# Performance work log

Hardware: AMD Instinct MI355X
Metric: run time of the kernel (lower is better)

## Reference

```python
import jax, jax.numpy as jnp
import numpy as np

B, S, H, E, K = 4, 4096, 1024, 8, 2
DFF = 4 * H


def setup_inputs() -> dict:
    key = jax.random.key(0)
    ks = jax.random.split(key, 6)
    s_in = 1.0 / np.sqrt(H)
    s_ff = 1.0 / np.sqrt(DFF)
    return {
        "x": jax.random.normal(ks[0], (B, S, H), dtype=jnp.float32),
        "router_w": jax.random.normal(ks[1], (E, H), dtype=jnp.float32) * s_in,
        "router_b": jnp.zeros((E,), dtype=jnp.float32),
        "fc1_w": jax.random.normal(ks[2], (E, DFF, H), dtype=jnp.float32) * s_in,
        "fc1_b": jnp.zeros((E, DFF), dtype=jnp.float32),
        "fc2_w": jax.random.normal(ks[3], (E, H, DFF), dtype=jnp.float32) * s_ff,
        "fc2_b": jnp.zeros((E, H), dtype=jnp.float32),
    }


def reference(x, router_w, router_b, fc1_w, fc1_b, fc2_w, fc2_b):
    b, s, h = x.shape
    e = router_w.shape[0]
    k = K
    # Router: [B,S,E]
    logits = jnp.einsum("bsh,eh->bse", x, router_w) + router_b
    top_v, top_i = jax.lax.top_k(logits, k)            # [B,S,K]
    probs = jax.nn.softmax(top_v, axis=-1)             # softmax over top-k logits
    # Combine weights per expert [B,S,E]; top-k indices are distinct per token,
    # so summing one-hot*prob over k matches the original's gather-of-first-match.
    combine = jnp.sum(jax.nn.one_hot(top_i, e, dtype=x.dtype) * probs[..., None], axis=-2)
    xf = x.reshape(-1, h)            # [T,H], T = B*S
    cf = combine.reshape(-1, e)      # [T,E]
    out = jnp.zeros_like(xf)
    for ei in range(e):              # fixed small loop over experts
        hdn = jax.nn.relu(xf @ fc1_w[ei].T + fc1_b[ei])   # [T,4H]
        y = hdn @ fc2_w[ei].T + fc2_b[ei]                 # [T,H]
        out = out + cf[:, ei:ei + 1] * y                  # zero weight == not routed
    return out.reshape(b, s, h)
```

## Files before the change

### kernel.cpp

```cpp
#include <hip/hip_runtime.h>
#include <stdint.h>

#define T_TOKENS 16384
#define H_DIM 1024
#define E_NUM 8
#define DFF_DIM 4096

#define BMT 128
#define BNT 128
#define BKT 64
#define MT_CAP 264
#define PAD_ROWS (MT_CAP * BMT)
#define NCHUNK 4
#define MT_PER_CHUNK (MT_CAP / NCHUNK)
#define CHUNK_ROWS (MT_PER_CHUNK * BMT)

#define WS_COUNTS     0
#define WS_CURSOR     32
#define WS_OFFS       64
#define WS_SLOT_TOK   256
#define WS_SLOT_W     135424
#define WS_EIDX       270592
#define WS_EW         401664
#define WS_WC1        532736
#define WS_WC2        67641600
#define WS_XB         134750464
#define WS_HDN        168304896
#define WS_OUTK1      237510912
#define WS_REQUIRED   271065344UL
#define WS_SMALL_ZERO 270592

typedef __attribute__((ext_vector_type(8))) short short8;
typedef __attribute__((ext_vector_type(4))) float f32x4;

__device__ __forceinline__ unsigned short f2bf(float f) {
  union { float f; unsigned int u; } v; v.f = f;
  unsigned int r = v.u + 0x7FFFu + ((v.u >> 16) & 1u);
  return (unsigned short)(r >> 16);
}

__device__ __forceinline__ float bf2f(unsigned short b) {
  union { unsigned int u; float f; } v; v.u = ((unsigned int)b) << 16;
  return v.f;
}

__device__ __forceinline__ void load_lds16(const void* g, void* l) {
  __builtin_amdgcn_global_load_lds(
      (const __attribute__((address_space(1))) void*)g,
      (__attribute__((address_space(3))) void*)l, 16, 0, 0);
}

#define CONV_BLOCKS 2048
__global__ __launch_bounds__(256) void convert_weights(
    const float* __restrict__ w1, const float* __restrict__ w2,
    unsigned short* __restrict__ wc1, unsigned short* __restrict__ wc2) {
  const int total4 = (E_NUM * DFF_DIM * H_DIM) / 4;
  const int step = CONV_BLOCKS * 256;
  for (int i = blockIdx.x * 256 + threadIdx.x; i < total4; i += step) {
    float4 a = ((const float4*)w1)[i];
    float4 b = ((const float4*)w2)[i];
    ushort4 ua, ub;
    ua.x = f2bf(a.x); ua.y = f2bf(a.y); ua.z = f2bf(a.z); ua.w = f2bf(a.w);
    ub.x = f2bf(b.x); ub.y = f2bf(b.y); ub.z = f2bf(b.z); ub.w = f2bf(b.w);
    ((ushort4*)wc1)[i] = ua;
    ((ushort4*)wc2)[i] = ub;
  }
}

__global__ __launch_bounds__(256) void router_kernel(
    const float* __restrict__ x, const float* __restrict__ rw,
    const float* __restrict__ rb, unsigned short* __restrict__ xb,
    int* __restrict__ eidx, float* __restrict__ ew) {
  __shared__ float4 rws[E_NUM * 256];
  const int tid = threadIdx.x;
#pragma unroll
  for (int k = 0; k < 8; ++k) rws[k * 256 + tid] = ((const float4*)rw)[k * 256 + tid];
  __syncthreads();

  const int wave = tid >> 6;
  const int lane = tid & 63;
#pragma unroll
  for (int i = 0; i < 4; ++i) {
    const int t = blockIdx.x * 16 + wave * 4 + i;
    const float4* xrow = (const float4*)(x + (size_t)t * H_DIM);
    float4 xv[4];
#pragma unroll
    for (int j = 0; j < 4; ++j) xv[j] = xrow[j * 64 + lane];

    ushort4* xbrow = (ushort4*)(xb + (size_t)t * H_DIM);
#pragma unroll
    for (int j = 0; j < 4; ++j) {
      ushort4 o;
      o.x = f2bf(xv[j].x); o.y = f2bf(xv[j].y);
      o.z = f2bf(xv[j].z); o.w = f2bf(xv[j].w);
      xbrow[j * 64 + lane] = o;
    }

    float s[E_NUM];
#pragma unroll
    for (int e = 0; e < E_NUM; ++e) {
      float a = 0.f;
#pragma unroll
      for (int j = 0; j < 4; ++j) {
        float4 wv = rws[e * 256 + j * 64 + lane];
        a += xv[j].x * wv.x + xv[j].y * wv.y + xv[j].z * wv.z + xv[j].w * wv.w;
      }
      s[e] = a;
    }
#pragma unroll
    for (int off = 32; off; off >>= 1) {
#pragma unroll
      for (int e = 0; e < E_NUM; ++e) s[e] += __shfl_xor(s[e], off);
    }
    if (lane == 0) {
      float lg[E_NUM];
#pragma unroll
      for (int e = 0; e < E_NUM; ++e) lg[e] = s[e] + rb[e];
      int i0 = 0; float m0 = lg[0];
#pragma unroll
      for (int e = 1; e < E_NUM; ++e)
        if (lg[e] > m0) { m0 = lg[e]; i0 = e; }
      int i1 = -1; float m1 = -3.4e38f;
#pragma unroll
      for (int e = 0; e < E_NUM; ++e)
        if (e != i0 && lg[e] > m1) { m1 = lg[e]; i1 = e; }
      float e1 = expf(m1 - m0);
      float denom = 1.f + e1;
      ((int2*)eidx)[t] = make_int2(i0, i1);
      ((float2*)ew)[t] = make_float2(1.f / denom, e1 / denom);
    }
  }
}

__global__ __launch_bounds__(1024) void count_kernel(const int* __restrict__ eidx,
                                                     int* __restrict__ counts,
                                                     int* __restrict__ offs,
                                                     int* __restrict__ cursor) {
  __shared__ int hist[E_NUM];
  const int tid = threadIdx.x;
  const int lane = tid & 63;
  if (tid < E_NUM) hist[tid] = 0;
  __syncthreads();
  int c[E_NUM];
#pragma unroll
  for (int e = 0; e < E_NUM; ++e) c[e] = 0;
  const int4* p = (const int4*)eidx;
#pragma unroll
  for (int i = 0; i < 8; ++i) {
    int4 v = p[i * 1024 + tid];
#pragma unroll
    for (int e = 0; e < E_NUM; ++e)
      c[e] += (v.x == e) + (v.y == e) + (v.z == e) + (v.w == e);
  }
#pragma unroll
  for (int off = 32; off; off >>= 1) {
#pragma unroll
    for (int e = 0; e < E_NUM; ++e) c[e] += __shfl_xor(c[e], off);
  }
  if (lane == 0) {
#pragma unroll
    for (int e = 0; e < E_NUM; ++e) atomicAdd(&hist[e], c[e]);
  }
  __syncthreads();
  if (tid == 0) {
    int acc = 0;
    offs[0] = 0;
#pragma unroll
    for (int e = 0; e < E_NUM; ++e) {
      counts[e] = hist[e];
      cursor[e] = 0;
      acc += ((hist[e] + BMT - 1) / BMT) * BMT;
      offs[e + 1] = acc;
    }
  }
}

__global__ __launch_bounds__(1024) void scatter_kernel(
    const int* __restrict__ eidx, const float* __restrict__ ew,
    const int* __restrict__ offs, int* __restrict__ cursor,
    int* __restrict__ slot_token, float* __restrict__ slot_w) {
  __shared__ int wcnt[16][E_NUM];
  __shared__ int wpre[16][E_NUM];
  __shared__ int bbase[E_NUM];
  __shared__ int soffs[E_NUM];
  const int tid = threadIdx.x, w = tid >> 6, lane = tid & 63;
  const int t = blockIdx.x * 1024 + tid;
  const int2 epair = ((const int2*)eidx)[t];
  const float2 wpair = ((const float2*)ew)[t];
  const int e0 = epair.x, e1 = epair.y;
  const unsigned long long lt = (1ULL << lane) - 1ULL;
  if (tid < E_NUM) soffs[tid] = offs[tid];
  int r0 = 0, r1 = 0;
#pragma unroll
  for (int e = 0; e < E_NUM; ++e) {
    unsigned long long m0 = __ballot(e0 == e);
    unsigned long long m1 = __ballot(e1 == e);
    int c0 = __popcll(m0);
    if (e0 == e) r0 = __popcll(m0 & lt);
    if (e1 == e) r1 = c0 + __popcll(m1 & lt);
    if (lane == 0) wcnt[w][e] = c0 + __popcll(m1);
  }
  __syncthreads();
  if (tid < E_NUM) {
    int run = 0;
#pragma unroll
    for (int w2 = 0; w2 < 16; ++w2) {
      wpre[w2][tid] = run;
      run += wcnt[w2][tid];
    }
    bbase[tid] = atomicAdd(&cursor[tid], run);
  }
  __syncthreads();
  const int s0 = soffs[e0] + bbase[e0] + wpre[w][e0] + r0;
  const int s1 = soffs[e1] + bbase[e1] + wpre[w][e1] + r1;
  slot_token[s0] = t;
  slot_w[s0] = wpair.x;
  slot_token[s1] = t | (int)0x80000000;
  slot_w[s1] = wpair.y;
}

template <int KTOT>
__device__ __forceinline__ void gemm_core(const unsigned short* const* aptr,
                                          const unsigned short* const* bptr,
                                          unsigned short* lA, unsigned short* lB,
                                          f32x4 acc[4][4]) {
  const int tid = threadIdx.x;
  const int w = tid >> 6, lane = tid & 63;
  const int wm = w >> 1, wn = w & 1;
  const int rrow = lane & 15;
  const int rq = lane >> 4;

  for (int ks = 0; ks < KTOT / BKT; ++ks) {
    const int k0 = ks * BKT;
#pragma unroll
    for (int i = 0; i < 4; ++i) {
      load_lds16(aptr[i] + k0, lA + i * 2048 + w * 512);
      load_lds16(bptr[i] + k0, lB + i * 2048 + w * 512);
    }
    __syncthreads();
#pragma unroll
    for (int kk = 0; kk < 2; ++kk) {
      short8 af[4], bfr[4];
#pragma unroll
      for (int mi = 0; mi < 4; ++mi)
        af[mi] = *(const short8*)(lA + (wm * 64 + mi * 16 + rrow) * BKT + kk * 32 + rq * 8);
#pragma unroll
      for (int ni = 0; ni < 4; ++ni)
        bfr[ni] = *(const short8*)(lB + (wn * 64 + ni * 16 + rrow) * BKT + kk * 32 + rq * 8);
#pragma unroll
      for (int mi = 0; mi < 4; ++mi)
#pragma unroll
        for (int ni = 0; ni < 4; ++ni)
          acc[mi][ni] = __builtin_amdgcn_mfma_f32_16x16x32_bf16(af[mi], bfr[ni], acc[mi][ni], 0, 0, 0);
    }
    __syncthreads();
  }
}

__global__ __launch_bounds__(256, 2) void fc1_kernel(
    const unsigned short* __restrict__ xb, const unsigned short* __restrict__ wc1,
    const float* __restrict__ fc1_b, const int* __restrict__ offs,
    const int* __restrict__ counts, const int* __restrict__ slot_token,
    unsigned short* __restrict__ hdn, int chunk) {
  __shared__ unsigned short sA[BMT * BKT];
  __shared__ unsigned short sB[BNT * BKT];
  const int mt = chunk * MT_PER_CHUNK + blockIdx.y;
  const int row0 = mt * BMT;
  if (row0 >= offs[E_NUM]) return;
  int e = 0;
#pragma unroll
  for (int i = 1; i < E_NUM; ++i) e = (row0 >= offs[i]) ? i : e;
  const int n0 = blockIdx.x * BNT;

  f32x4 acc[4][4];
  f32x4 zf = {0.f, 0.f, 0.f, 0.f};
#pragma unroll
  for (int mi = 0; mi < 4; ++mi)
#pragma unroll
    for (int ni = 0; ni < 4; ++ni) acc[mi][ni] = zf;

  const int tid = threadIdx.x;
  const int srow = tid >> 3;
  const int scol = (tid & 7) * 8;
  const unsigned short* Bm = wc1 + (size_t)e * DFF_DIM * H_DIM + (size_t)n0 * H_DIM;
  const unsigned short* aptr[4];
  const unsigned short* bptr[4];
#pragma unroll
  for (int i = 0; i < 4; ++i) {
    const int r = i * 32 + srow;
    const int tok = slot_token[row0 + r] & 0x7FFFFFFF;
    aptr[i] = xb + (size_t)tok * H_DIM + scol;
    bptr[i] = Bm + (size_t)r * H_DIM + scol;
  }
  gemm_core<H_DIM>(aptr, bptr, sA, sB, acc);

  const int w = tid >> 6;
  const int lane = tid & 63;
  const int wm = w >> 1, wn = w & 1;
  const int rrow = lane & 15, rq = lane >> 4;
  const int cnt = counts[e];
  const int lbase = row0 - offs[e];
  const int hrow0 = row0 - chunk * CHUNK_ROWS;
#pragma unroll
  for (int mi = 0; mi < 4; ++mi) {
#pragma unroll
    for (int j = 0; j < 4; ++j) {
      const int rit = wm * 64 + mi * 16 + rq * 4 + j;
      if (lbase + rit >= cnt) continue;
      unsigned short* hrow = hdn + (size_t)(hrow0 + rit) * DFF_DIM;
#pragma unroll
      for (int ni = 0; ni < 4; ++ni) {
        const int n = n0 + wn * 64 + ni * 16 + rrow;
        float v = acc[mi][ni][j] + fc1_b[e * DFF_DIM + n];
        v = v > 0.f ? v : 0.f;
        hrow[n] = f2bf(v);
      }
    }
  }
}

__global__ __launch_bounds__(256, 2) void fc2_kernel(
    const unsigned short* __restrict__ hdn, const unsigned short* __restrict__ wc2,
    const float* __restrict__ fc2_b, const int* __restrict__ offs,
    const int* __restrict__ counts, const int* __restrict__ slot_token,
    const float* __restrict__ slot_w, float* __restrict__ out,
    unsigned short* __restrict__ outk1, int chunk) {
  __shared__ unsigned short sA[BMT * BKT];
  __shared__ unsigned short sB[BNT * BKT];
  const int id = blockIdx.x;
  const int xcd = id & 7, j = id >> 3;
  int ml, nt;
  if (j < 64) { ml = xcd * 8 + (j & 7); nt = j >> 3; }
  else        { ml = 64 + (j & 1);      nt = xcd;    }
  const int mt = chunk * MT_PER_CHUNK + ml;
  const int row0 = mt * BMT;
  if (row0 >= offs[E_NUM]) return;
  int e = 0;
#pragma unroll
  for (int i = 1; i < E_NUM; ++i) e = (row0 >= offs[i]) ? i : e;
  const int n0 = nt * BNT;

  f32x4 acc[4][4];
  f32x4 zf = {0.f, 0.f, 0.f, 0.f};
#pragma unroll
  for (int mi = 0; mi < 4; ++mi)
#pragma unroll
    for (int ni = 0; ni < 4; ++ni) acc[mi][ni] = zf;

  const int tid = threadIdx.x;
  const int srow = tid >> 3;
  const int scol = (tid & 7) * 8;
  const unsigned short* A = hdn + (size_t)(ml * BMT) * DFF_DIM;
  const unsigned short* Bm = wc2 + (size_t)e * H_DIM * DFF_DIM + (size_t)n0 * DFF_DIM;
  const unsigned short* aptr[4];
  const unsigned short* bptr[4];
#pragma unroll
  for (int i = 0; i < 4; ++i) {
    const int r = i * 32 + srow;
    aptr[i] = A + (size_t)r * DFF_DIM + scol;
    bptr[i] = Bm + (size_t)r * DFF_DIM + scol;
  }
  gemm_core<DFF_DIM>(aptr, bptr, sA, sB, acc);

  const int w = tid >> 6;
  const int lane = tid & 63;
  const int wm = w >> 1, wn = w & 1;
  const int rrow = lane & 15, rq = lane >> 4;
  const int cnt = counts[e];
  const int lbase = row0 - offs[e];
#pragma unroll
  for (int mi = 0; mi < 4; ++mi) {
#pragma unroll
    for (int j2 = 0; j2 < 4; ++j2) {
      const int rit = wm * 64 + mi * 16 + rq * 4 + j2;
      if (lbase + rit >= cnt) continue;
      const int gr = row0 + rit;
      const int st = slot_token[gr];
      const int tok = st & 0x7FFFFFFF;
      const float wgt = slot_w[gr];
#pragma unroll
      for (int ni = 0; ni < 4; ++ni) {
        const int h = n0 + wn * 64 + ni * 16 + rrow;
        const float v = (acc[mi][ni][j2] + fc2_b[e * H_DIM + h]) * wgt;
        if (st >= 0) out[(size_t)tok * H_DIM + h] = v;
        else         outk1[(size_t)tok * H_DIM + h] = f2bf(v);
      }
    }
  }
}

__global__ __launch_bounds__(256) void add_kernel(
    float* __restrict__ out, const unsigned short* __restrict__ outk1) {
  const int wave = threadIdx.x >> 6;
  const int lane = threadIdx.x & 63;
  const int t = blockIdx.x * 4 + wave;
  float4* orow = (float4*)(out + (size_t)t * H_DIM);
  const ushort4* krow = (const ushort4*)(outk1 + (size_t)t * H_DIM);
#pragma unroll
  for (int j = 0; j < 4; ++j) {
    const int idx = j * 64 + lane;
    float4 a = orow[idx];
    ushort4 b = krow[idx];
    a.x += bf2f(b.x); a.y += bf2f(b.y); a.z += bf2f(b.z); a.w += bf2f(b.w);
    orow[idx] = a;
  }
}

extern "C" void kernel_launch(void* const* d_in, const int* in_sizes, int n_in,
                              void* d_out, int out_size, void* d_ws, size_t ws_size,
                              hipStream_t stream) {
  const float* x        = (const float*)d_in[0];
  const float* router_w = (const float*)d_in[1];
  const float* router_b = (const float*)d_in[2];
  const float* fc1_w    = (const float*)d_in[3];
  const float* fc1_b    = (const float*)d_in[4];
  const float* fc2_w    = (const float*)d_in[5];
  const float* fc2_b    = (const float*)d_in[6];
  float* out = (float*)d_out;

  char* ws = (char*)d_ws;
  int* counts            = (int*)(ws + WS_COUNTS);
  int* cursor            = (int*)(ws + WS_CURSOR);
  int* offs              = (int*)(ws + WS_OFFS);
  int* slot_token        = (int*)(ws + WS_SLOT_TOK);
  float* slot_w          = (float*)(ws + WS_SLOT_W);
  int* eidx              = (int*)(ws + WS_EIDX);
  float* ew              = (float*)(ws + WS_EW);
  unsigned short* wc1    = (unsigned short*)(ws + WS_WC1);
  unsigned short* wc2    = (unsigned short*)(ws + WS_WC2);
  unsigned short* xb     = (unsigned short*)(ws + WS_XB);
  unsigned short* hdn    = (unsigned short*)(ws + WS_HDN);
  unsigned short* outk1  = (unsigned short*)(ws + WS_OUTK1);

  if (ws_size < WS_REQUIRED) {
    hipMemsetAsync(d_out, 0, (size_t)T_TOKENS * H_DIM * sizeof(float), stream);
    return;
  }
  hipMemsetAsync(ws, 0, WS_SMALL_ZERO, stream);

  convert_weights<<<CONV_BLOCKS, 256, 0, stream>>>(fc1_w, fc2_w, wc1, wc2);
  router_kernel<<<T_TOKENS / 16, 256, 0, stream>>>(x, router_w, router_b, xb, eidx, ew);
  count_kernel<<<1, 1024, 0, stream>>>(eidx, counts, offs, cursor);
  scatter_kernel<<<T_TOKENS / 1024, 1024, 0, stream>>>(eidx, ew, offs, cursor, slot_token, slot_w);

  for (int c = 0; c < NCHUNK; ++c) {
    fc1_kernel<<<dim3(DFF_DIM / BNT, MT_PER_CHUNK), 256, 0, stream>>>(
        xb, wc1, fc1_b, offs, counts, slot_token, hdn, c);
    fc2_kernel<<<8 * MT_PER_CHUNK, 256, 0, stream>>>(
        hdn, wc2, fc2_b, offs, counts, slot_token, slot_w, out, outk1, c);
  }
  add_kernel<<<T_TOKENS / 4, 256, 0, stream>>>(out, outk1);
}
```

Measured before the change: 1.049 ms.

## Use 256-row double-buffered fc2 tiles with 512 threads and drop slot_w

fc2 now uses 256x128 output tiles computed by 512 threads (8 waves) with double-buffered LDS staging, so each weight tile is reused across twice as many rows and global loads overlap MFMA work. Expert padding is raised to 256 rows to fit the larger tile, and chunk sizing is recomputed to match. The per-slot weight array is removed and the weight is gathered from ew by token index. The costs are extra padded rows, double the LDS per block, and lower occupancy.

```diff
diff --git a/kernel.cpp b/kernel.cpp
--- a/kernel.cpp
+++ b/kernel.cpp
@@ -9,26 +9,25 @@
 #define BMT 128
 #define BNT 128
 #define BKT 64
-#define MT_CAP 264
-#define PAD_ROWS (MT_CAP * BMT)
 #define NCHUNK 4
-#define MT_PER_CHUNK (MT_CAP / NCHUNK)
-#define CHUNK_ROWS (MT_PER_CHUNK * BMT)
+#define MT1_PER_CHUNK 68
+#define MT2_PER_CHUNK 34
+#define CHUNK_ROWS 8704
+#define PAD_MAX (NCHUNK * CHUNK_ROWS)
 
 #define WS_COUNTS     0
 #define WS_CURSOR     32
 #define WS_OFFS       64
 #define WS_SLOT_TOK   256
-#define WS_SLOT_W     135424
-#define WS_EIDX       270592
-#define WS_EW         401664
-#define WS_WC1        532736
-#define WS_WC2        67641600
-#define WS_XB         134750464
-#define WS_HDN        168304896
-#define WS_OUTK1      237510912
-#define WS_REQUIRED   271065344UL
-#define WS_SMALL_ZERO 270592
+#define WS_EIDX       139520
+#define WS_EW         270592
+#define WS_WC1        401664
+#define WS_WC2        67510528
+#define WS_XB         134619392
+#define WS_HDN        168173824
+#define WS_OUTK1      239476992
+#define WS_REQUIRED   273031424UL
+#define WS_SMALL_ZERO 139520
 
 typedef __attribute__((ext_vector_type(8))) short short8;
 typedef __attribute__((ext_vector_type(4))) float f32x4;
@@ -169,16 +168,15 @@
     for (int e = 0; e < E_NUM; ++e) {
       counts[e] = hist[e];
       cursor[e] = 0;
-      acc += ((hist[e] + BMT - 1) / BMT) * BMT;
+      acc += ((hist[e] + 255) / 256) * 256;
       offs[e + 1] = acc;
     }
   }
 }
 
 __global__ __launch_bounds__(1024) void scatter_kernel(
-    const int* __restrict__ eidx, const float* __restrict__ ew,
-    const int* __restrict__ offs, int* __restrict__ cursor,
-    int* __restrict__ slot_token, float* __restrict__ slot_w) {
+    const int* __restrict__ eidx, const int* __restrict__ offs,
+    int* __restrict__ cursor, int* __restrict__ slot_token) {
   __shared__ int wcnt[16][E_NUM];
   __shared__ int wpre[16][E_NUM];
   __shared__ int bbase[E_NUM];
@@ -186,7 +184,6 @@
   const int tid = threadIdx.x, w = tid >> 6, lane = tid & 63;
   const int t = blockIdx.x * 1024 + tid;
   const int2 epair = ((const int2*)eidx)[t];
-  const float2 wpair = ((const float2*)ew)[t];
   const int e0 = epair.x, e1 = epair.y;
   const unsigned long long lt = (1ULL << lane) - 1ULL;
   if (tid < E_NUM) soffs[tid] = offs[tid];
@@ -214,9 +211,7 @@
   const int s0 = soffs[e0] + bbase[e0] + wpre[w][e0] + r0;
   const int s1 = soffs[e1] + bbase[e1] + wpre[w][e1] + r1;
   slot_token[s0] = t;
-  slot_w[s0] = wpair.x;
   slot_token[s1] = t | (int)0x80000000;
-  slot_w[s1] = wpair.y;
 }
 
 template <int KTOT>
@@ -264,8 +259,7 @@
     unsigned short* __restrict__ hdn, int chunk) {
   __shared__ unsigned short sA[BMT * BKT];
   __shared__ unsigned short sB[BNT * BKT];
-  const int mt = chunk * MT_PER_CHUNK + blockIdx.y;
-  const int row0 = mt * BMT;
+  const int row0 = chunk * CHUNK_ROWS + blockIdx.y * BMT;
   if (row0 >= offs[E_NUM]) return;
   int e = 0;
 #pragma unroll
@@ -319,26 +313,27 @@
   }
 }
 
-__global__ __launch_bounds__(256, 2) void fc2_kernel(
+__global__ __launch_bounds__(512, 2) void fc2_kernel(
     const unsigned short* __restrict__ hdn, const unsigned short* __restrict__ wc2,
     const float* __restrict__ fc2_b, const int* __restrict__ offs,
     const int* __restrict__ counts, const int* __restrict__ slot_token,
-    const float* __restrict__ slot_w, float* __restrict__ out,
+    const float* __restrict__ ew, float* __restrict__ out,
     unsigned short* __restrict__ outk1, int chunk) {
-  __shared__ unsigned short sA[BMT * BKT];
-  __shared__ unsigned short sB[BNT * BKT];
+  __shared__ unsigned short sA0[256 * 64];
+  __shared__ unsigned short sB0[128 * 64];
+  __shared__ unsigned short sA1[256 * 64];
+  __shared__ unsigned short sB1[128 * 64];
   const int id = blockIdx.x;
   const int xcd = id & 7, j = id >> 3;
-  int ml, nt;
-  if (j < 64) { ml = xcd * 8 + (j & 7); nt = j >> 3; }
-  else        { ml = 64 + (j & 1);      nt = xcd;    }
-  const int mt = chunk * MT_PER_CHUNK + ml;
-  const int row0 = mt * BMT;
+  const int g = xcd * MT2_PER_CHUNK + j;
+  const int ml = g >> 3;
+  const int nt = g & 7;
+  const int row0 = chunk * CHUNK_ROWS + ml * 256;
   if (row0 >= offs[E_NUM]) return;
   int e = 0;
 #pragma unroll
   for (int i = 1; i < E_NUM; ++i) e = (row0 >= offs[i]) ? i : e;
-  const int n0 = nt * BNT;
+  const int n0 = nt * 128;
 
   f32x4 acc[4][4];
   f32x4 zf = {0.f, 0.f, 0.f, 0.f};
@@ -348,24 +343,69 @@
     for (int ni = 0; ni < 4; ++ni) acc[mi][ni] = zf;
 
   const int tid = threadIdx.x;
+  const int w = tid >> 6, lane = tid & 63;
+  const int wm = w >> 1, wn = w & 1;
+  const int rrow = lane & 15, rq = lane >> 4;
   const int srow = tid >> 3;
   const int scol = (tid & 7) * 8;
-  const unsigned short* A = hdn + (size_t)(ml * BMT) * DFF_DIM;
+  const unsigned short* A = hdn + (size_t)(ml * 256) * DFF_DIM;
   const unsigned short* Bm = wc2 + (size_t)e * H_DIM * DFF_DIM + (size_t)n0 * DFF_DIM;
   const unsigned short* aptr[4];
-  const unsigned short* bptr[4];
-#pragma unroll
-  for (int i = 0; i < 4; ++i) {
-    const int r = i * 32 + srow;
-    aptr[i] = A + (size_t)r * DFF_DIM + scol;
-    bptr[i] = Bm + (size_t)r * DFF_DIM + scol;
-  }
-  gemm_core<DFF_DIM>(aptr, bptr, sA, sB, acc);
-
-  const int w = tid >> 6;
-  const int lane = tid & 63;
-  const int wm = w >> 1, wn = w & 1;
-  const int rrow = lane & 15, rq = lane >> 4;
+  const unsigned short* bptr[2];
+#pragma unroll
+  for (int i = 0; i < 4; ++i)
+    aptr[i] = A + (size_t)(i * 64 + srow) * DFF_DIM + scol;
+#pragma unroll
+  for (int i = 0; i < 2; ++i)
+    bptr[i] = Bm + (size_t)(i * 64 + srow) * DFF_DIM + scol;
+
+#define FC2_STAGE(DA, DB, K0)                                        \
+  {                                                                  \
+    _Pragma("unroll")                                                \
+    for (int i = 0; i < 4; ++i)                                      \
+      load_lds16(aptr[i] + (K0), (DA) + i * 4096 + w * 512);         \
+    _Pragma("unroll")                                                \
+    for (int i = 0; i < 2; ++i)                                      \
+      load_lds16(bptr[i] + (K0), (DB) + i * 4096 + w * 512);         \
+  }
+
+#define FC2_COMPUTE(SA, SB)                                                         \
+  {                                                                                 \
+    _Pragma("unroll")                                                               \
+    for (int kk = 0; kk < 2; ++kk) {                                                \
+      short8 af[4], bfr[4];                                                         \
+      _Pragma("unroll")                                                             \
+      for (int mi = 0; mi < 4; ++mi)                                                \
+        af[mi] = *(const short8*)((SA) + (wm * 64 + mi * 16 + rrow) * BKT + kk * 32 + rq * 8); \
+      _Pragma("unroll")                                                             \
+      for (int ni = 0; ni < 4; ++ni)                                                \
+        bfr[ni] = *(const short8*)((SB) + (wn * 64 + ni * 16 + rrow) * BKT + kk * 32 + rq * 8); \
+      _Pragma("unroll")                                                             \
+      for (int mi = 0; mi < 4; ++mi)                                                \
+        _Pragma("unroll")                                                           \
+        for (int ni = 0; ni < 4; ++ni)                                              \
+          acc[mi][ni] = __builtin_amdgcn_mfma_f32_16x16x32_bf16(af[mi], bfr[ni], acc[mi][ni], 0, 0, 0); \
+    }                                                                               \
+  }
+
+  FC2_STAGE(sA0, sB0, 0)
+  __syncthreads();
+  for (int ks = 0; ks < 62; ks += 2) {
+    FC2_STAGE(sA1, sB1, (ks + 1) * BKT)
+    FC2_COMPUTE(sA0, sB0)
+    __syncthreads();
+    FC2_STAGE(sA0, sB0, (ks + 2) * BKT)
+    FC2_COMPUTE(sA1, sB1)
+    __syncthreads();
+  }
+  FC2_STAGE(sA1, sB1, 63 * BKT)
+  FC2_COMPUTE(sA0, sB0)
+  __syncthreads();
+  FC2_COMPUTE(sA1, sB1)
+
+#undef FC2_STAGE
+#undef FC2_COMPUTE
+
   const int cnt = counts[e];
   const int lbase = row0 - offs[e];
 #pragma unroll
@@ -377,7 +417,7 @@
       const int gr = row0 + rit;
       const int st = slot_token[gr];
       const int tok = st & 0x7FFFFFFF;
-      const float wgt = slot_w[gr];
+      const float wgt = ew[2 * tok + (st < 0 ? 1 : 0)];
 #pragma unroll
       for (int ni = 0; ni < 4; ++ni) {
         const int h = n0 + wn * 64 + ni * 16 + rrow;
@@ -423,7 +463,6 @@
   int* cursor            = (int*)(ws + WS_CURSOR);
   int* offs              = (int*)(ws + WS_OFFS);
   int* slot_token        = (int*)(ws + WS_SLOT_TOK);
-  float* slot_w          = (float*)(ws + WS_SLOT_W);
   int* eidx              = (int*)(ws + WS_EIDX);
   float* ew              = (float*)(ws + WS_EW);
   unsigned short* wc1    = (unsigned short*)(ws + WS_WC1);
@@ -441,13 +480,13 @@
   convert_weights<<<CONV_BLOCKS, 256, 0, stream>>>(fc1_w, fc2_w, wc1, wc2);
   router_kernel<<<T_TOKENS / 16, 256, 0, stream>>>(x, router_w, router_b, xb, eidx, ew);
   count_kernel<<<1, 1024, 0, stream>>>(eidx, counts, offs, cursor);
-  scatter_kernel<<<T_TOKENS / 1024, 1024, 0, stream>>>(eidx, ew, offs, cursor, slot_token, slot_w);
+  scatter_kernel<<<T_TOKENS / 1024, 1024, 0, stream>>>(eidx, offs, cursor, slot_token);
 
   for (int c = 0; c < NCHUNK; ++c) {
-    fc1_kernel<<<dim3(DFF_DIM / BNT, MT_PER_CHUNK), 256, 0, stream>>>(
+    fc1_kernel<<<dim3(DFF_DIM / BNT, MT1_PER_CHUNK), 256, 0, stream>>>(
         xb, wc1, fc1_b, offs, counts, slot_token, hdn, c);
-    fc2_kernel<<<8 * MT_PER_CHUNK, 256, 0, stream>>>(
-        hdn, wc2, fc2_b, offs, counts, slot_token, slot_w, out, outk1, c);
+    fc2_kernel<<<8 * MT2_PER_CHUNK, 512, 0, stream>>>(
+        hdn, wc2, fc2_b, offs, counts, slot_token, ew, out, outk1, c);
   }
   add_kernel<<<T_TOKENS / 4, 256, 0, stream>>>(out, outk1);
 }
```

Measured after the change: 1.479 ms. 1.41x slower.
